# Performance work log

Hardware: AMD Instinct MI355X
Metric: run time of the kernel (lower is better)

The kernel has to match this reference:

```python
import jax, jax.numpy as jnp
import numpy as np

N = 50000        # nodes
E = 800000       # edges
IN_DIM, HID, OUT = 512, 256, 128
EPS = 1e-5       # PyG LayerNorm eps (added to std)


def setup_inputs() -> dict:
    key = jax.random.key(0)
    ks = jax.random.split(key, 24)
    def lin(k, i, o, scale=0.05):
        kw, kb = jax.random.split(k)
        return (jax.random.normal(kw, (i, o), jnp.float32) * scale,
                jax.random.normal(kb, (o,), jnp.float32) * scale)
    x = jax.random.normal(ks[0], (N, IN_DIM), jnp.float32)
    edge_index = jax.random.randint(ks[1], (2, E), 0, N, jnp.int64)
    Wq1, bq1 = lin(ks[2], IN_DIM, HID)
    Wk1, bk1 = lin(ks[3], IN_DIM, HID)
    Wv1, bv1 = lin(ks[4], IN_DIM, HID)
    Ws1, bs1 = lin(ks[5], IN_DIM, HID)
    g1 = jnp.ones((HID,), jnp.float32)
    be1 = jnp.zeros((HID,), jnp.float32)
    Wq2, bq2 = lin(ks[6], HID, OUT)
    Wk2, bk2 = lin(ks[7], HID, OUT)
    Wv2, bv2 = lin(ks[8], HID, OUT)
    Ws2, bs2 = lin(ks[9], HID, OUT)
    g2 = jnp.ones((OUT,), jnp.float32)
    be2 = jnp.zeros((OUT,), jnp.float32)
    return dict(x=x, Wq1=Wq1, bq1=bq1, Wk1=Wk1, bk1=bk1, Wv1=Wv1, bv1=bv1,
                Ws1=Ws1, bs1=bs1, g1=g1, be1=be1,
                Wq2=Wq2, bq2=bq2, Wk2=Wk2, bk2=bk2, Wv2=Wv2, bv2=bv2,
                Ws2=Ws2, bs2=bs2, g2=g2, be2=be2, edge_index=edge_index)


def transformer_conv(x, edge_index, Wq, bq, Wk, bk, Wv, bv, Ws, bs):
    # PyG TransformerConv, heads=1, concat=True, root_weight=True
    src, dst = edge_index[0], edge_index[1]
    n = x.shape[0]
    d = Wq.shape[1]
    q = x @ Wq + bq                               # [N, d]
    k = x @ Wk + bk
    v = x @ Wv + bv
    score = (q[dst] * k[src]).sum(-1) / jnp.sqrt(jnp.asarray(d, x.dtype))  # [E]
    m = jax.ops.segment_max(score, dst, num_segments=n)     # per-target max
    e = jnp.exp(score - m[dst])
    denom = jax.ops.segment_sum(e, dst, num_segments=n)
    alpha = e / denom[dst]                         # scatter-softmax over in-edges
    agg = jax.ops.segment_sum(alpha[:, None] * v[src], dst, num_segments=n)
    return agg + (x @ Ws + bs)                     # root/skip connection


def graph_layer_norm(h, w, b):
    # PyG LayerNorm mode='graph', no batch: normalize over ALL entries
    h = h - h.mean()
    return h / (h.std() + EPS) * w + b


def reference(x, Wq1, bq1, Wk1, bk1, Wv1, bv1, Ws1, bs1, g1, be1,
              Wq2, bq2, Wk2, bk2, Wv2, bv2, Ws2, bs2, g2, be2, edge_index):
    a1 = graph_layer_norm(
        transformer_conv(x, edge_index, Wq1, bq1, Wk1, bk1, Wv1, bv1, Ws1, bs1),
        g1, be1)
    h1 = jax.nn.elu(a1)  # ELU(alpha=1.0)
    h2 = graph_layer_norm(
        transformer_conv(h1, edge_index, Wq2, bq2, Wk2, bk2, Wv2, bv2, Ws2, bs2),
        g2, be2)
    return h2
```

## Files before the change

### kernel.cpp

```cpp
#include <hip/hip_runtime.h>
#include <stdint.h>
#include <math.h>

#define IN_DIM 512
#define HID    256
#define OUTD   128
#define LN_EPS 1e-5f
#define NSLOT  2048

typedef unsigned short u16;
typedef unsigned int   u32;
typedef short short8 __attribute__((ext_vector_type(8)));
typedef float f32x4  __attribute__((ext_vector_type(4)));

__device__ __forceinline__ float bf2f(u32 h) {
  union { u32 u; float f; } c; c.u = h << 16; return c.f;
}
__device__ __forceinline__ u16 f2bf(float f) {
  union { float f; u32 u; } c; c.f = f;
  u32 u = c.u;
  return (u16)((u + 0x7FFFu + ((u >> 16) & 1u)) >> 16);
}

__device__ __forceinline__ void gload_lds16(const void* g, void* l) {
  __builtin_amdgcn_global_load_lds((const __attribute__((address_space(1))) void*)g,
                                   (__attribute__((address_space(3))) void*)l, 16, 0, 0);
}

__global__ __launch_bounds__(256) void k_prep(
    const float* __restrict__ x, u16* __restrict__ x_bf, int n4,
    const int* __restrict__ edst, int* __restrict__ deg, int E,
    const float* __restrict__ bq1, const float* __restrict__ bk1,
    const float* __restrict__ bv1, const float* __restrict__ bs1,
    const float* __restrict__ bq2, const float* __restrict__ bk2,
    const float* __restrict__ bv2, const float* __restrict__ bs2,
    float* __restrict__ bc1, float* __restrict__ bc2,
    const float* __restrict__ Wq1, const float* __restrict__ Wk1,
    const float* __restrict__ Wv1, const float* __restrict__ Ws1,
    const float* __restrict__ Wq2, const float* __restrict__ Wk2,
    const float* __restrict__ Wv2, const float* __restrict__ Ws2,
    u16* __restrict__ Wt1, u16* __restrict__ Wt2,
    int b_cvt, int b_hist) {
  __shared__ u16 t[32][33];
  int blk = blockIdx.x;
  int tid = threadIdx.x;
  if (blk < b_cvt) {
    int id = blk * 256 + tid;
    if (id < n4) {
      const float4 v = ((const float4*)x)[id];
      ushort4 o;
      o.x = f2bf(v.x); o.y = f2bf(v.y); o.z = f2bf(v.z); o.w = f2bf(v.w);
      ((ushort4*)x_bf)[id] = o;
    }
    return;
  }
  blk -= b_cvt;
  if (blk < b_hist) {
    int e = blk * 256 + tid;
    if (e < E) atomicAdd(&deg[edst[e]], 1);
    return;
  }
  blk -= b_hist;
  if (blk < 6) {
    int id = blk * 256 + tid;
    if (id < 4 * HID) {
      const float* s = (id < HID) ? bq1 : (id < 2 * HID) ? bk1 : (id < 3 * HID) ? bv1 : bs1;
      bc1[id] = s[id & (HID - 1)];
    } else if (id < 4 * HID + 4 * OUTD) {
      int j = id - 4 * HID;
      const float* s = (j < OUTD) ? bq2 : (j < 2 * OUTD) ? bk2 : (j < 3 * OUTD) ? bv2 : bs2;
      bc2[j] = s[j & (OUTD - 1)];
    }
    return;
  }
  blk -= 6;
  int tx = tid & 31, ty = tid >> 5;
  if (blk < 512) {
    int mat = blk >> 7, r = blk & 127;
    int k0 = (r >> 3) * 32, n0 = (r & 7) * 32;
    const float* src = (mat == 0) ? Wq1 : (mat == 1) ? Wk1 : (mat == 2) ? Wv1 : Ws1;
    u16* dst = Wt1 + (size_t)mat * IN_DIM * HID;
#pragma unroll
    for (int i = 0; i < 32; i += 8)
      t[ty + i][tx] = f2bf(src[(size_t)(k0 + ty + i) * HID + n0 + tx]);
    __syncthreads();
#pragma unroll
    for (int i = 0; i < 32; i += 8)
      dst[(size_t)(n0 + ty + i) * IN_DIM + k0 + tx] = t[tx][ty + i];
    return;
  }
  blk -= 512;
  {
    int mat = blk >> 5, r = blk & 31;
    int k0 = (r >> 2) * 32, n0 = (r & 3) * 32;
    const float* src = (mat == 0) ? Wq2 : (mat == 1) ? Wk2 : (mat == 2) ? Wv2 : Ws2;
    u16* dst = Wt2 + (size_t)mat * HID * OUTD;
#pragma unroll
    for (int i = 0; i < 32; i += 8)
      t[ty + i][tx] = f2bf(src[(size_t)(k0 + ty + i) * OUTD + n0 + tx]);
    __syncthreads();
#pragma unroll
    for (int i = 0; i < 32; i += 8)
      dst[(size_t)(n0 + ty + i) * HID + k0 + tx] = t[tx][ty + i];
  }
}

__global__ void k_block_sum(const int* __restrict__ deg, int* __restrict__ bsum, int n) {
  __shared__ int sm[256];
  int i = blockIdx.x * 256 + threadIdx.x;
  sm[threadIdx.x] = (i < n) ? deg[i] : 0;
  __syncthreads();
  for (int off = 128; off > 0; off >>= 1) {
    if (threadIdx.x < off) sm[threadIdx.x] += sm[threadIdx.x + off];
    __syncthreads();
  }
  if (threadIdx.x == 0) bsum[blockIdx.x] = sm[0];
}

__global__ void k_scan_bsum(const int* __restrict__ bsum, int* __restrict__ boff, int nb) {
  __shared__ int sm[256];
  int t = threadIdx.x;
  int v = (t < nb) ? bsum[t] : 0;
  sm[t] = v;
  __syncthreads();
  for (int off = 1; off < 256; off <<= 1) {
    int tmp = (t >= off) ? sm[t - off] : 0;
    __syncthreads();
    sm[t] += tmp;
    __syncthreads();
  }
  if (t < nb) boff[t] = sm[t] - v;
}

__global__ void k_scan_final(const int* __restrict__ deg, const int* __restrict__ boff,
                             int* __restrict__ offsets, int* __restrict__ cur,
                             int n, int total) {
  __shared__ int sm[256];
  int t = threadIdx.x;
  int i = blockIdx.x * 256 + t;
  int v = (i < n) ? deg[i] : 0;
  sm[t] = v;
  __syncthreads();
  for (int off = 1; off < 256; off <<= 1) {
    int tmp = (t >= off) ? sm[t - off] : 0;
    __syncthreads();
    sm[t] += tmp;
    __syncthreads();
  }
  if (i < n) {
    int o = boff[blockIdx.x] + sm[t] - v;
    offsets[i] = o;
    cur[i] = o;
  }
  if (i == 0) offsets[n] = total;
}

__global__ void k_scatter(const int* __restrict__ src, const int* __restrict__ dst,
                          int* __restrict__ cursor, int* __restrict__ ssrc, int E) {
  int e = blockIdx.x * blockDim.x + threadIdx.x;
  if (e >= E) return;
  int d = dst[e];
  int pos = atomicAdd(&cursor[d], 1);
  ssrc[pos] = src[e];
}

__global__ __launch_bounds__(256, 2) void k_gemm_bf16_nt(
    const u16* __restrict__ A, const u16* __restrict__ Bt, const float* __restrict__ bias,
    u16* __restrict__ C, int M, int K, int Nt) {
  __shared__ __align__(16) u16 As[128 * 32];
  __shared__ __align__(16) u16 Bs[256 * 32];
  const int tid = threadIdx.x;
  const int bm0 = blockIdx.x * 128;
  const int bn0 = blockIdx.y * 256;
  const int wave = tid >> 6, lane = tid & 63;
  const int q = lane >> 4, r16 = lane & 15;
  const int wm = (wave >> 1) * 64;
  const int wn = (wave & 1) * 128;

  f32x4 acc[4][8];
#pragma unroll
  for (int i = 0; i < 4; i++)
#pragma unroll
    for (int j = 0; j < 8; j++) acc[i][j] = (f32x4){0.f, 0.f, 0.f, 0.f};

  for (int kt = 0; kt < K; kt += 32) {
#pragma unroll
    for (int j = 0; j < 2; ++j) {
      int t = j * 256 + tid;
      gload_lds16(A + (size_t)(bm0 + (t >> 2)) * K + kt + (t & 3) * 8, &As[t * 8]);
    }
#pragma unroll
    for (int j = 0; j < 4; ++j) {
      int t = j * 256 + tid;
      gload_lds16(Bt + (size_t)(bn0 + (t >> 2)) * K + kt + (t & 3) * 8, &Bs[t * 8]);
    }
    __syncthreads();
    short8 bfr[8];
#pragma unroll
    for (int j = 0; j < 8; ++j)
      bfr[j] = *(const short8*)(&Bs[(wn + j * 16 + r16) * 32 + q * 8]);
#pragma unroll
    for (int i = 0; i < 4; ++i) {
      short8 af = *(const short8*)(&As[(wm + i * 16 + r16) * 32 + q * 8]);
#pragma unroll
      for (int j = 0; j < 8; ++j)
        acc[i][j] = __builtin_amdgcn_mfma_f32_16x16x32_bf16(af, bfr[j], acc[i][j], 0, 0, 0);
    }
    __syncthreads();
  }

#pragma unroll
  for (int i = 0; i < 4; i++) {
#pragma unroll
    for (int r = 0; r < 4; r++) {
      int grow = bm0 + wm + i * 16 + q * 4 + r;
      if (grow >= M) continue;
      size_t rbase = (size_t)grow * Nt;
#pragma unroll
      for (int j = 0; j < 8; j++) {
        int gcol = bn0 + wn + j * 16 + r16;
        float v = acc[i][j][r] + bias[gcol];
        C[rbase + gcol] = f2bf(v);
      }
    }
  }
}

template <int VPL>
__device__ __forceinline__ void load_bf(const u16* __restrict__ p, int lane, float* f) {
  if constexpr (VPL == 4) {
    uint2 r = *(const uint2*)(p + lane * 4);
    f[0] = bf2f(r.x & 0xffffu); f[1] = bf2f(r.x >> 16);
    f[2] = bf2f(r.y & 0xffffu); f[3] = bf2f(r.y >> 16);
  } else {
    u32 r = *(const u32*)(p + lane * 2);
    f[0] = bf2f(r & 0xffffu); f[1] = bf2f(r >> 16);
  }
}

template <int H, bool OUT_BF16>
__global__ __launch_bounds__(256) void k_conv(
    const u16* __restrict__ qkvs, const int* __restrict__ offsets,
    const int* __restrict__ ssrc, u16* __restrict__ out_bf,
    float* __restrict__ out_f, int n, float scale,
    float* __restrict__ ssum, float* __restrict__ ssq) {
  constexpr int VPL = H / 64;
  int gw = (blockIdx.x * blockDim.x + threadIdx.x) >> 6;
  int wave = threadIdx.x >> 6;
  int lane = threadIdx.x & 63;
  if (gw >= n) return;
  const u16* base = qkvs + (size_t)gw * (4 * H);
  float qf[VPL];
  load_bf<VPL>(base, lane, qf);
  int beg = offsets[gw], end = offsets[gw + 1];
  float m = -INFINITY, l = 0.f;
  float agg[VPL];
#pragma unroll
  for (int w = 0; w < VPL; w++) agg[w] = 0.f;

  int i = beg;
  for (; i + 4 <= end; i += 4) {
    int s0 = ssrc[i], s1 = ssrc[i + 1], s2 = ssrc[i + 2], s3 = ssrc[i + 3];
    const u16* k0p = qkvs + (size_t)s0 * (4 * H) + H;
    const u16* k1p = qkvs + (size_t)s1 * (4 * H) + H;
    const u16* k2p = qkvs + (size_t)s2 * (4 * H) + H;
    const u16* k3p = qkvs + (size_t)s3 * (4 * H) + H;
    float k0[VPL], k1[VPL], k2[VPL], k3[VPL];
    float v0[VPL], v1[VPL], v2[VPL], v3[VPL];
    load_bf<VPL>(k0p, lane, k0);
    load_bf<VPL>(k1p, lane, k1);
    load_bf<VPL>(k2p, lane, k2);
    load_bf<VPL>(k3p, lane, k3);
    load_bf<VPL>(k0p + H, lane, v0);
    load_bf<VPL>(k1p + H, lane, v1);
    load_bf<VPL>(k2p + H, lane, v2);
    load_bf<VPL>(k3p + H, lane, v3);
    float d0 = 0.f, d1 = 0.f, d2 = 0.f, d3 = 0.f;
#pragma unroll
    for (int w = 0; w < VPL; w++) {
      d0 += qf[w] * k0[w]; d1 += qf[w] * k1[w];
      d2 += qf[w] * k2[w]; d3 += qf[w] * k3[w];
    }
#pragma unroll
    for (int off = 32; off > 0; off >>= 1) {
      d0 += __shfl_xor(d0, off, 64);
      d1 += __shfl_xor(d1, off, 64);
      d2 += __shfl_xor(d2, off, 64);
      d3 += __shfl_xor(d3, off, 64);
    }
    d0 *= scale; d1 *= scale; d2 *= scale; d3 *= scale;
    float cm = fmaxf(fmaxf(d0, d1), fmaxf(d2, d3));
    float nm = fmaxf(m, cm);
    float sc = __expf(m - nm);
    float p0 = __expf(d0 - nm), p1 = __expf(d1 - nm);
    float p2 = __expf(d2 - nm), p3 = __expf(d3 - nm);
    m = nm;
    l = l * sc + (p0 + p1) + (p2 + p3);
#pragma unroll
    for (int w = 0; w < VPL; w++)
      agg[w] = agg[w] * sc + p0 * v0[w] + p1 * v1[w] + p2 * v2[w] + p3 * v3[w];
  }
  for (; i < end; ++i) {
    int s = ssrc[i];
    const u16* kb = qkvs + (size_t)s * (4 * H) + H;
    float kf[VPL], vf[VPL];
    load_bf<VPL>(kb, lane, kf);
    load_bf<VPL>(kb + H, lane, vf);
    float d = 0.f;
#pragma unroll
    for (int w = 0; w < VPL; w++) d += qf[w] * kf[w];
#pragma unroll
    for (int off = 32; off > 0; off >>= 1) d += __shfl_xor(d, off, 64);
    float score = d * scale;
    float nm = fmaxf(m, score);
    float sc = __expf(m - nm);
    float p = __expf(score - nm);
    m = nm;
    l = l * sc + p;
#pragma unroll
    for (int w = 0; w < VPL; w++) agg[w] = agg[w] * sc + p * vf[w];
  }

  float sf[VPL];
  load_bf<VPL>(base + 3 * H, lane, sf);
  float inv = (end > beg) ? 1.f / l : 0.f;
  float r[VPL];
#pragma unroll
  for (int w = 0; w < VPL; w++) {
    r[w] = agg[w] * inv + sf[w];
    if (OUT_BF16) out_bf[(size_t)gw * H + lane * VPL + w] = f2bf(r[w]);
    else out_f[(size_t)gw * H + lane * VPL + w] = r[w];
  }

  float s = 0.f, s2 = 0.f;
#pragma unroll
  for (int w = 0; w < VPL; w++) { s += r[w]; s2 += r[w] * r[w]; }
#pragma unroll
  for (int off = 32; off > 0; off >>= 1) {
    s += __shfl_xor(s, off, 64);
    s2 += __shfl_xor(s2, off, 64);
  }
  if (lane == 0) {
    int slot = (blockIdx.x * 4 + wave) & (NSLOT - 1);
    atomicAdd(&ssum[slot], s);
    atomicAdd(&ssq[slot], s2);
  }
}

__device__ __forceinline__ void slot_stats(const float* __restrict__ ssum,
                                           const float* __restrict__ ssq,
                                           double cnt, float& mu, float& inv) {
  __shared__ double rs[256], rq[256];
  double ls = 0.0, lq = 0.0;
  for (int i = threadIdx.x; i < NSLOT; i += 256) {
    ls += (double)ssum[i];
    lq += (double)ssq[i];
  }
  rs[threadIdx.x] = ls; rq[threadIdx.x] = lq;
  __syncthreads();
  for (int off = 128; off > 0; off >>= 1) {
    if (threadIdx.x < off) { rs[threadIdx.x] += rs[threadIdx.x + off]; rq[threadIdx.x] += rq[threadIdx.x + off]; }
    __syncthreads();
  }
  double mud = rs[0] / cnt;
  double var = rq[0] / cnt - mud * mud;
  if (var < 0.0) var = 0.0;
  mu = (float)mud;
  inv = (float)(1.0 / (sqrt(var) + (double)LN_EPS));
}

__global__ __launch_bounds__(256) void k_norm_elu_bf16(
    const u16* __restrict__ a, const float* __restrict__ g,
    const float* __restrict__ b, const float* __restrict__ ssum,
    const float* __restrict__ ssq, double cnt,
    u16* __restrict__ out, int n8, int Hmask) {
  float mu, inv;
  slot_stats(ssum, ssq, cnt, mu, inv);
  int id = blockIdx.x * blockDim.x + threadIdx.x;
  if (id >= n8) return;
  int i8 = id * 8;
  int cb = i8 & Hmask;
  uint4 v = *(const uint4*)(a + i8);
  const u32 va[4] = {v.x, v.y, v.z, v.w};
  uint4 o;
  u32* op = (u32*)&o;
#pragma unroll
  for (int w = 0; w < 4; w++) {
    float y0 = (bf2f(va[w] & 0xffffu) - mu) * inv * g[cb + 2 * w] + b[cb + 2 * w];
    float y1 = (bf2f(va[w] >> 16) - mu) * inv * g[cb + 2 * w + 1] + b[cb + 2 * w + 1];
    y0 = (y0 > 0.f) ? y0 : (__expf(y0) - 1.f);
    y1 = (y1 > 0.f) ? y1 : (__expf(y1) - 1.f);
    op[w] = (u32)f2bf(y0) | ((u32)f2bf(y1) << 16);
  }
  *(uint4*)(out + i8) = o;
}

__global__ __launch_bounds__(256) void k_norm_f32(
    float* __restrict__ a, const float* __restrict__ g,
    const float* __restrict__ b, const float* __restrict__ ssum,
    const float* __restrict__ ssq, double cnt, int n4, int Hmask) {
  float mu, inv;
  slot_stats(ssum, ssq, cnt, mu, inv);
  int id = blockIdx.x * blockDim.x + threadIdx.x;
  if (id >= n4) return;
  int i4 = id * 4;
  int cb = i4 & Hmask;
  float4 v = *(const float4*)(a + i4);
  float4 o;
  o.x = (v.x - mu) * inv * g[cb] + b[cb];
  o.y = (v.y - mu) * inv * g[cb + 1] + b[cb + 1];
  o.z = (v.z - mu) * inv * g[cb + 2] + b[cb + 2];
  o.w = (v.w - mu) * inv * g[cb + 3] + b[cb + 3];
  *(float4*)(a + i4) = o;
}

extern "C" void kernel_launch(void* const* d_in, const int* in_sizes, int n_in,
                              void* d_out, int out_size, void* d_ws, size_t ws_size,
                              hipStream_t stream) {
  const float* x   = (const float*)d_in[0];
  const float* Wq1 = (const float*)d_in[1];  const float* bq1 = (const float*)d_in[2];
  const float* Wk1 = (const float*)d_in[3];  const float* bk1 = (const float*)d_in[4];
  const float* Wv1 = (const float*)d_in[5];  const float* bv1 = (const float*)d_in[6];
  const float* Ws1 = (const float*)d_in[7];  const float* bs1 = (const float*)d_in[8];
  const float* g1  = (const float*)d_in[9];  const float* be1 = (const float*)d_in[10];
  const float* Wq2 = (const float*)d_in[11]; const float* bq2 = (const float*)d_in[12];
  const float* Wk2 = (const float*)d_in[13]; const float* bk2 = (const float*)d_in[14];
  const float* Wv2 = (const float*)d_in[15]; const float* bv2 = (const float*)d_in[16];
  const float* Ws2 = (const float*)d_in[17]; const float* bs2 = (const float*)d_in[18];
  const float* g2  = (const float*)d_in[19]; const float* be2 = (const float*)d_in[20];
  const int*   ei  = (const int*)d_in[21];

  const int N = in_sizes[0] / IN_DIM;
  const int E = in_sizes[21] / 2;
  const int* esrc = ei;
  const int* edst = ei + E;

  char* w = (char*)d_ws;
  auto carve = [&](size_t bytes) { char* p = w; w += (bytes + 255) & ~(size_t)255; return p; };
  int* deg     = (int*)carve((size_t)(N + 1) * 4);
  float* slots = (float*)carve(4 * NSLOT * 4);
  u16* x_bf  = (u16*)carve((size_t)N * IN_DIM * 2);
  u16* Wt1   = (u16*)carve((size_t)4 * HID * IN_DIM * 2);
  u16* Wt2   = (u16*)carve((size_t)4 * OUTD * HID * 2);
  float* bc1 = (float*)carve(4 * HID * 4);
  float* bc2 = (float*)carve(4 * OUTD * 4);
  u16* qkvs1 = (u16*)carve((size_t)N * 4 * HID * 2);
  u16* a1    = (u16*)carve((size_t)N * HID * 2);
  int* offs  = (int*)carve((size_t)(N + 1) * 4);
  int* cur   = (int*)carve((size_t)(N + 1) * 4);
  int* ssrc  = (int*)carve((size_t)E * 4);
  int* bsum  = (int*)carve(1024);
  int* boff  = (int*)carve(1024);
  u16* h1    = x_bf;
  u16* qkvs2 = qkvs1;
  float* ssum1 = slots, *ssq1 = slots + NSLOT;
  float* ssum2 = slots + 2 * NSLOT, *ssq2 = slots + 3 * NSLOT;

  hipMemsetAsync(deg, 0, (size_t)((char*)(slots + 4 * NSLOT) - (char*)deg), stream);

  int n4 = N * IN_DIM / 4;
  int b_cvt = (n4 + 255) / 256;
  int b_hist = (E + 255) / 256;
  int k1_blocks = b_cvt + b_hist + 6 + 512 + 128;
  k_prep<<<k1_blocks, 256, 0, stream>>>(
      x, x_bf, n4, edst, deg, E,
      bq1, bk1, bv1, bs1, bq2, bk2, bv2, bs2, bc1, bc2,
      Wq1, Wk1, Wv1, Ws1, Wq2, Wk2, Wv2, Ws2, Wt1, Wt2, b_cvt, b_hist);

  int nb = (N + 255) / 256;
  k_block_sum<<<nb, 256, 0, stream>>>(deg, bsum, N);
  k_scan_bsum<<<1, 256, 0, stream>>>(bsum, boff, nb);
  k_scan_final<<<nb, 256, 0, stream>>>(deg, boff, offs, cur, N, E);

  k_scatter<<<b_hist, 256, 0, stream>>>(esrc, edst, cur, ssrc, E);

  dim3 gg1((N + 127) / 128, (4 * HID) / 256);
  k_gemm_bf16_nt<<<gg1, 256, 0, stream>>>(x_bf, Wt1, bc1, qkvs1, N, IN_DIM, 4 * HID);

  k_conv<HID, true><<<(N + 3) / 4, 256, 0, stream>>>(qkvs1, offs, ssrc, a1, nullptr, N,
                                                     1.0f / sqrtf((float)HID), ssum1, ssq1);
  k_norm_elu_bf16<<<N * HID / 8 / 256, 256, 0, stream>>>(
      a1, g1, be1, ssum1, ssq1, (double)N * HID, h1, N * HID / 8, HID - 1);

  dim3 gg2((N + 127) / 128, (4 * OUTD) / 256);
  k_gemm_bf16_nt<<<gg2, 256, 0, stream>>>(h1, Wt2, bc2, qkvs2, N, HID, 4 * OUTD);

  k_conv<OUTD, false><<<(N + 3) / 4, 256, 0, stream>>>(qkvs2, offs, ssrc, nullptr, (float*)d_out,
                                                       N, 1.0f / sqrtf((float)OUTD), ssum2, ssq2);
  k_norm_f32<<<N * OUTD / 4 / 256, 256, 0, stream>>>(
      (float*)d_out, g2, be2, ssum2, ssq2, (double)N * OUTD, N * OUTD / 4, OUTD - 1);
}
```

Measured before the change: 622.9 us.

## Quantize gathered K/V to int8 per-node and fuse edge scatter into GEMM launch

The GEMM epilogue now splits its output into separate Q/S and K/V buffers. A new quantization kernel converts K (and V in layer 1) to int8 with a per-node, per-section scale. The conv kernels gather these int8 rows instead of bf16, which halves the bytes read per edge in the bandwidth-bound attention aggregation. The CSR edge scatter is folded into the layer-1 GEMM launch as extra blocks, removing one kernel launch. This trades accuracy for less gather traffic and adds extra quantize passes plus a wider output write.

```diff
diff --git a/kernel.cpp b/kernel.cpp
--- a/kernel.cpp
+++ b/kernel.cpp
@@ -10,6 +10,7 @@
 
 typedef unsigned short u16;
 typedef unsigned int   u32;
+typedef unsigned char  u8;
 typedef short short8 __attribute__((ext_vector_type(8)));
 typedef float f32x4  __attribute__((ext_vector_type(4)));
 
@@ -20,6 +21,10 @@
   union { float f; u32 u; } c; c.f = f;
   u32 u = c.u;
   return (u16)((u + 0x7FFFu + ((u >> 16) & 1u)) >> 16);
+}
+template <int W>
+__device__ __forceinline__ float i8f(u32 word) {
+  return (float)((int)(word << (24 - 8 * W)) >> 24);
 }
 
 __device__ __forceinline__ void gload_lds16(const void* g, void* l) {
@@ -155,23 +160,27 @@
   if (i == 0) offsets[n] = total;
 }
 
-__global__ void k_scatter(const int* __restrict__ src, const int* __restrict__ dst,
-                          int* __restrict__ cursor, int* __restrict__ ssrc, int E) {
-  int e = blockIdx.x * blockDim.x + threadIdx.x;
-  if (e >= E) return;
-  int d = dst[e];
-  int pos = atomicAdd(&cursor[d], 1);
-  ssrc[pos] = src[e];
-}
-
-__global__ __launch_bounds__(256, 2) void k_gemm_bf16_nt(
+__global__ __launch_bounds__(256, 2) void k_gemm(
     const u16* __restrict__ A, const u16* __restrict__ Bt, const float* __restrict__ bias,
-    u16* __restrict__ C, int M, int K, int Nt) {
+    u16* __restrict__ Cb, u16* __restrict__ Ck,
+    int M, int K, int Nt, int mbx, int cklo, int ckhi, int sB, int sK,
+    int gemm_blocks,
+    const int* __restrict__ esrc, const int* __restrict__ edst,
+    int* __restrict__ cur, int* __restrict__ ssrc, int E) {
+  if ((int)blockIdx.x >= gemm_blocks) {
+    int e = (blockIdx.x - gemm_blocks) * 256 + threadIdx.x;
+    if (e < E) {
+      int d = edst[e];
+      int pos = atomicAdd(&cur[d], 1);
+      ssrc[pos] = esrc[e];
+    }
+    return;
+  }
   __shared__ __align__(16) u16 As[128 * 32];
   __shared__ __align__(16) u16 Bs[256 * 32];
   const int tid = threadIdx.x;
-  const int bm0 = blockIdx.x * 128;
-  const int bn0 = blockIdx.y * 256;
+  const int bm0 = (blockIdx.x % mbx) * 128;
+  const int bn0 = (blockIdx.x / mbx) * 256;
   const int wave = tid >> 6, lane = tid & 63;
   const int q = lane >> 4, r16 = lane & 15;
   const int wm = (wave >> 1) * 64;
@@ -209,78 +218,133 @@
     __syncthreads();
   }
 
+  const int wk = ckhi - cklo;
 #pragma unroll
   for (int i = 0; i < 4; i++) {
 #pragma unroll
     for (int r = 0; r < 4; r++) {
       int grow = bm0 + wm + i * 16 + q * 4 + r;
       if (grow >= M) continue;
-      size_t rbase = (size_t)grow * Nt;
 #pragma unroll
       for (int j = 0; j < 8; j++) {
         int gcol = bn0 + wn + j * 16 + r16;
         float v = acc[i][j][r] + bias[gcol];
-        C[rbase + gcol] = f2bf(v);
+        if (gcol < cklo) Cb[(size_t)grow * sB + gcol] = f2bf(v);
+        else if (gcol < ckhi) Ck[(size_t)grow * sK + gcol - cklo] = f2bf(v);
+        else Cb[(size_t)grow * sB + gcol - wk] = f2bf(v);
       }
     }
   }
 }
 
-template <int VPL>
-__device__ __forceinline__ void load_bf(const u16* __restrict__ p, int lane, float* f) {
+template <int SECW, int NSEC>
+__global__ __launch_bounds__(256) void k_quant(
+    const u16* __restrict__ src, u8* __restrict__ dst,
+    float* __restrict__ sc, int n) {
+  constexpr int VPL = SECW / 64;
+  int gw = (blockIdx.x * blockDim.x + threadIdx.x) >> 6;
+  int lane = threadIdx.x & 63;
+  int node = gw / NSEC, sec = gw - node * NSEC;
+  if (node >= n) return;
+  const u16* p = src + (size_t)node * (NSEC * SECW) + sec * SECW + lane * VPL;
+  float f[VPL];
   if constexpr (VPL == 4) {
-    uint2 r = *(const uint2*)(p + lane * 4);
+    uint2 r = *(const uint2*)p;
     f[0] = bf2f(r.x & 0xffffu); f[1] = bf2f(r.x >> 16);
     f[2] = bf2f(r.y & 0xffffu); f[3] = bf2f(r.y >> 16);
   } else {
-    u32 r = *(const u32*)(p + lane * 2);
+    u32 r = *(const u32*)p;
     f[0] = bf2f(r & 0xffffu); f[1] = bf2f(r >> 16);
   }
-}
-
-template <int H, bool OUT_BF16>
+  float amax = 0.f;
+#pragma unroll
+  for (int w = 0; w < VPL; w++) amax = fmaxf(amax, fabsf(f[w]));
+#pragma unroll
+  for (int off = 32; off > 0; off >>= 1) amax = fmaxf(amax, __shfl_xor(amax, off, 64));
+  float rs = (amax > 0.f) ? 127.0f / amax : 0.f;
+  u32 packed = 0;
+#pragma unroll
+  for (int w = 0; w < VPL; w++) {
+    int qv = (int)rintf(f[w] * rs);
+    packed |= ((u32)(qv & 0xff)) << (8 * w);
+  }
+  u8* d = dst + (size_t)node * (NSEC * SECW) + sec * SECW + lane * VPL;
+  if constexpr (VPL == 4) *(u32*)d = packed;
+  else *(u16*)d = (u16)packed;
+  if (lane == 0) sc[node * NSEC + sec] = amax / 127.0f;
+}
+
+template <int H, bool OUT_BF16, bool V_I8>
 __global__ __launch_bounds__(256) void k_conv(
-    const u16* __restrict__ qkvs, const int* __restrict__ offsets,
-    const int* __restrict__ ssrc, u16* __restrict__ out_bf,
-    float* __restrict__ out_f, int n, float scale,
+    const u16* __restrict__ qs, const u8* __restrict__ k8,
+    const float* __restrict__ sc,
+    const int* __restrict__ offsets, const int* __restrict__ ssrc,
+    u16* __restrict__ out_bf, float* __restrict__ out_f, int n, float scale,
     float* __restrict__ ssum, float* __restrict__ ssq) {
   constexpr int VPL = H / 64;
+  constexpr int QSTR = V_I8 ? 2 * H : 3 * H;
+  constexpr int SOFF = V_I8 ? H : 2 * H;
+  constexpr int KSTR = V_I8 ? 2 * H : H;
   int gw = (blockIdx.x * blockDim.x + threadIdx.x) >> 6;
   int wave = threadIdx.x >> 6;
   int lane = threadIdx.x & 63;
   if (gw >= n) return;
-  const u16* base = qkvs + (size_t)gw * (4 * H);
+  const u16* base = qs + (size_t)gw * QSTR;
   float qf[VPL];
-  load_bf<VPL>(base, lane, qf);
+  if constexpr (VPL == 4) {
+    uint2 rq = *(const uint2*)(base + lane * 4);
+    qf[0] = bf2f(rq.x & 0xffffu); qf[1] = bf2f(rq.x >> 16);
+    qf[2] = bf2f(rq.y & 0xffffu); qf[3] = bf2f(rq.y >> 16);
+  } else {
+    u32 rq = *(const u32*)(base + lane * 2);
+    qf[0] = bf2f(rq & 0xffffu); qf[1] = bf2f(rq >> 16);
+  }
   int beg = offsets[gw], end = offsets[gw + 1];
   float m = -INFINITY, l = 0.f;
   float agg[VPL];
 #pragma unroll
   for (int w = 0; w < VPL; w++) agg[w] = 0.f;
 
+  auto kload = [&](int s) -> u32 {
+    const u8* kp = k8 + (size_t)s * KSTR;
+    if constexpr (VPL == 4) return *(const u32*)(kp + lane * 4);
+    else return (u32)*(const u16*)(kp + lane * 2);
+  };
+  auto vload = [&](int s) -> u32 {
+    if constexpr (V_I8) return *(const u32*)(k8 + (size_t)s * KSTR + H + lane * 4);
+    else return *(const u32*)(qs + (size_t)s * QSTR + H + lane * 2);
+  };
+  auto vload2 = [&](int s) -> u32 {
+    return 0u;
+  };
+  (void)vload2;
+  auto dotk = [&](u32 kq) -> float {
+    float d = 0.f;
+    d += qf[0] * i8f<0>(kq);
+    d += qf[1] * i8f<1>(kq);
+    if constexpr (VPL == 4) {
+      d += qf[2] * i8f<2>(kq);
+      d += qf[3] * i8f<3>(kq);
+    }
+    return d;
+  };
+
   int i = beg;
   for (; i + 4 <= end; i += 4) {
     int s0 = ssrc[i], s1 = ssrc[i + 1], s2 = ssrc[i + 2], s3 = ssrc[i + 3];
-    const u16* k0p = qkvs + (size_t)s0 * (4 * H) + H;
-    const u16* k1p = qkvs + (size_t)s1 * (4 * H) + H;
-    const u16* k2p = qkvs + (size_t)s2 * (4 * H) + H;
-    const u16* k3p = qkvs + (size_t)s3 * (4 * H) + H;
-    float k0[VPL], k1[VPL], k2[VPL], k3[VPL];
-    float v0[VPL], v1[VPL], v2[VPL], v3[VPL];
-    load_bf<VPL>(k0p, lane, k0);
-    load_bf<VPL>(k1p, lane, k1);
-    load_bf<VPL>(k2p, lane, k2);
-    load_bf<VPL>(k3p, lane, k3);
-    load_bf<VPL>(k0p + H, lane, v0);
-    load_bf<VPL>(k1p + H, lane, v1);
-    load_bf<VPL>(k2p + H, lane, v2);
-    load_bf<VPL>(k3p + H, lane, v3);
-    float d0 = 0.f, d1 = 0.f, d2 = 0.f, d3 = 0.f;
-#pragma unroll
-    for (int w = 0; w < VPL; w++) {
-      d0 += qf[w] * k0[w]; d1 += qf[w] * k1[w];
-      d2 += qf[w] * k2[w]; d3 += qf[w] * k3[w];
-    }
+    u32 kq0 = kload(s0), kq1 = kload(s1), kq2 = kload(s2), kq3 = kload(s3);
+    u32 v0 = vload(s0), v1 = vload(s1), v2 = vload(s2), v3 = vload(s3);
+    float ks0, ks1, ks2, ks3, vs0, vs1, vs2, vs3;
+    if constexpr (V_I8) {
+      float2 a0 = *(const float2*)(sc + s0 * 2), a1 = *(const float2*)(sc + s1 * 2);
+      float2 a2 = *(const float2*)(sc + s2 * 2), a3 = *(const float2*)(sc + s3 * 2);
+      ks0 = a0.x; vs0 = a0.y; ks1 = a1.x; vs1 = a1.y;
+      ks2 = a2.x; vs2 = a2.y; ks3 = a3.x; vs3 = a3.y;
+    } else {
+      ks0 = sc[s0]; ks1 = sc[s1]; ks2 = sc[s2]; ks3 = sc[s3];
+      vs0 = vs1 = vs2 = vs3 = 1.f;
+    }
+    float d0 = dotk(kq0), d1 = dotk(kq1), d2 = dotk(kq2), d3 = dotk(kq3);
 #pragma unroll
     for (int off = 32; off > 0; off >>= 1) {
       d0 += __shfl_xor(d0, off, 64);
@@ -288,41 +352,74 @@
       d2 += __shfl_xor(d2, off, 64);
       d3 += __shfl_xor(d3, off, 64);
     }
-    d0 *= scale; d1 *= scale; d2 *= scale; d3 *= scale;
+    d0 *= scale * ks0; d1 *= scale * ks1; d2 *= scale * ks2; d3 *= scale * ks3;
     float cm = fmaxf(fmaxf(d0, d1), fmaxf(d2, d3));
     float nm = fmaxf(m, cm);
-    float sc = __expf(m - nm);
+    float sfac = __expf(m - nm);
     float p0 = __expf(d0 - nm), p1 = __expf(d1 - nm);
     float p2 = __expf(d2 - nm), p3 = __expf(d3 - nm);
     m = nm;
-    l = l * sc + (p0 + p1) + (p2 + p3);
-#pragma unroll
-    for (int w = 0; w < VPL; w++)
-      agg[w] = agg[w] * sc + p0 * v0[w] + p1 * v1[w] + p2 * v2[w] + p3 * v3[w];
+    l = l * sfac + (p0 + p1) + (p2 + p3);
+    if constexpr (V_I8) { p0 *= vs0; p1 *= vs1; p2 *= vs2; p3 *= vs3; }
+#pragma unroll
+    for (int w = 0; w < VPL; w++) {
+      float f0, f1, f2v, f3;
+      if constexpr (V_I8) {
+        f0 = (w == 0) ? i8f<0>(v0) : (w == 1) ? i8f<1>(v0) : (w == 2) ? i8f<2>(v0) : i8f<3>(v0);
+        f1 = (w == 0) ? i8f<0>(v1) : (w == 1) ? i8f<1>(v1) : (w == 2) ? i8f<2>(v1) : i8f<3>(v1);
+        f2v = (w == 0) ? i8f<0>(v2) : (w == 1) ? i8f<1>(v2) : (w == 2) ? i8f<2>(v2) : i8f<3>(v2);
+        f3 = (w == 0) ? i8f<0>(v3) : (w == 1) ? i8f<1>(v3) : (w == 2) ? i8f<2>(v3) : i8f<3>(v3);
+      } else {
+        u32 sh = 16 * (w & 1);
+        f0 = bf2f((v0 >> sh) & 0xffffu);
+        f1 = bf2f((v1 >> sh) & 0xffffu);
+        f2v = bf2f((v2 >> sh) & 0xffffu);
+        f3 = bf2f((v3 >> sh) & 0xffffu);
+      }
+      agg[w] = agg[w] * sfac + p0 * f0 + p1 * f1 + p2 * f2v + p3 * f3;
+    }
   }
   for (; i < end; ++i) {
     int s = ssrc[i];
-    const u16* kb = qkvs + (size_t)s * (4 * H) + H;
-    float kf[VPL], vf[VPL];
-    load_bf<VPL>(kb, lane, kf);
-    load_bf<VPL>(kb + H, lane, vf);
-    float d = 0.f;
-#pragma unroll
-    for (int w = 0; w < VPL; w++) d += qf[w] * kf[w];
+    u32 kq = kload(s);
+    u32 vr = vload(s);
+    float ks, vs;
+    if constexpr (V_I8) {
+      float2 a = *(const float2*)(sc + s * 2);
+      ks = a.x; vs = a.y;
+    } else { ks = sc[s]; vs = 1.f; }
+    float d = dotk(kq);
 #pragma unroll
     for (int off = 32; off > 0; off >>= 1) d += __shfl_xor(d, off, 64);
-    float score = d * scale;
+    float score = d * scale * ks;
     float nm = fmaxf(m, score);
-    float sc = __expf(m - nm);
+    float sfac = __expf(m - nm);
     float p = __expf(score - nm);
     m = nm;
-    l = l * sc + p;
-#pragma unroll
-    for (int w = 0; w < VPL; w++) agg[w] = agg[w] * sc + p * vf[w];
+    l = l * sfac + p;
+    float pv = V_I8 ? p * vs : p;
+#pragma unroll
+    for (int w = 0; w < VPL; w++) {
+      float vf;
+      if constexpr (V_I8)
+        vf = (w == 0) ? i8f<0>(vr) : (w == 1) ? i8f<1>(vr) : (w == 2) ? i8f<2>(vr) : i8f<3>(vr);
+      else vf = bf2f((vr >> (16 * (w & 1))) & 0xffffu);
+      agg[w] = agg[w] * sfac + pv * vf;
+    }
   }
 
   float sf[VPL];
-  load_bf<VPL>(base + 3 * H, lane, sf);
+  {
+    const u16* sp = base + SOFF;
+    if constexpr (VPL == 4) {
+      uint2 rs = *(const uint2*)(sp + lane * 4);
+      sf[0] = bf2f(rs.x & 0xffffu); sf[1] = bf2f(rs.x >> 16);
+      sf[2] = bf2f(rs.y & 0xffffu); sf[3] = bf2f(rs.y >> 16);
+    } else {
+      u32 rs = *(const u32*)(sp + lane * 2);
+      sf[0] = bf2f(rs & 0xffffu); sf[1] = bf2f(rs >> 16);
+    }
+  }
   float inv = (end > beg) ? 1.f / l : 0.f;
   float r[VPL];
 #pragma unroll
@@ -444,7 +541,10 @@
   u16* Wt2   = (u16*)carve((size_t)4 * OUTD * HID * 2);
   float* bc1 = (float*)carve(4 * HID * 4);
   float* bc2 = (float*)carve(4 * OUTD * 4);
-  u16* qkvs1 = (u16*)carve((size_t)N * 4 * HID * 2);
+  u16* qs1   = (u16*)carve((size_t)N * 2 * HID * 2);
+  u16* kvt   = (u16*)carve((size_t)N * 2 * HID * 2);
+  u8*  kv8   = (u8*)carve((size_t)N * 2 * HID);
+  float* sc1 = (float*)carve((size_t)N * 2 * 4);
   u16* a1    = (u16*)carve((size_t)N * HID * 2);
   int* offs  = (int*)carve((size_t)(N + 1) * 4);
   int* cur   = (int*)carve((size_t)(N + 1) * 4);
@@ -452,7 +552,10 @@
   int* bsum  = (int*)carve(1024);
   int* boff  = (int*)carve(1024);
   u16* h1    = x_bf;
-  u16* qkvs2 = qkvs1;
+  u16* qvs2  = qs1;
+  u16* ktmp2 = kvt;
+  u8*  k82   = kv8;
+  float* sc2 = sc1;
   float* ssum1 = slots, *ssq1 = slots + NSLOT;
   float* ssum2 = slots + 2 * NSLOT, *ssq2 = slots + 3 * NSLOT;
 
@@ -472,21 +575,33 @@
   k_scan_bsum<<<1, 256, 0, stream>>>(bsum, boff, nb);
   k_scan_final<<<nb, 256, 0, stream>>>(deg, boff, offs, cur, N, E);
 
-  k_scatter<<<b_hist, 256, 0, stream>>>(esrc, edst, cur, ssrc, E);
-
-  dim3 gg1((N + 127) / 128, (4 * HID) / 256);
-  k_gemm_bf16_nt<<<gg1, 256, 0, stream>>>(x_bf, Wt1, bc1, qkvs1, N, IN_DIM, 4 * HID);
-
-  k_conv<HID, true><<<(N + 3) / 4, 256, 0, stream>>>(qkvs1, offs, ssrc, a1, nullptr, N,
-                                                     1.0f / sqrtf((float)HID), ssum1, ssq1);
+  int mbx = (N + 127) / 128;
+  int g1_blocks = mbx * ((4 * HID) / 256);
+  k_gemm<<<g1_blocks + b_hist, 256, 0, stream>>>(
+      x_bf, Wt1, bc1, qs1, kvt, N, IN_DIM, 4 * HID, mbx,
+      HID, 3 * HID, 2 * HID, 2 * HID, g1_blocks,
+      esrc, edst, cur, ssrc, E);
+
+  k_quant<HID, 2><<<(N * 2 + 3) / 4, 256, 0, stream>>>(kvt, kv8, sc1, N);
+
+  k_conv<HID, true, true><<<(N + 3) / 4, 256, 0, stream>>>(
+      qs1, kv8, sc1, offs, ssrc, a1, nullptr, N, 1.0f / sqrtf((float)HID), ssum1, ssq1);
+
   k_norm_elu_bf16<<<N * HID / 8 / 256, 256, 0, stream>>>(
       a1, g1, be1, ssum1, ssq1, (double)N * HID, h1, N * HID / 8, HID - 1);
 
-  dim3 gg2((N + 127) / 128, (4 * OUTD) / 256);
-  k_gemm_bf16_nt<<<gg2, 256, 0, stream>>>(h1, Wt2, bc2, qkvs2, N, HID, 4 * OUTD);
-
-  k_conv<OUTD, false><<<(N + 3) / 4, 256, 0, stream>>>(qkvs2, offs, ssrc, nullptr, (float*)d_out,
-                                                       N, 1.0f / sqrtf((float)OUTD), ssum2, ssq2);
+  int g2_blocks = mbx * ((4 * OUTD) / 256);
+  k_gemm<<<g2_blocks, 256, 0, stream>>>(
+      h1, Wt2, bc2, qvs2, ktmp2, N, HID, 4 * OUTD, mbx,
+      OUTD, 2 * OUTD, 3 * OUTD, OUTD, g2_blocks,
+      nullptr, nullptr, nullptr, nullptr, 0);
+
+  k_quant<OUTD, 1><<<(N + 3) / 4, 256, 0, stream>>>(ktmp2, k82, sc2, N);
+
+  k_conv<OUTD, false, false><<<(N + 3) / 4, 256, 0, stream>>>(
+      qvs2, k82, sc2, offs, ssrc, nullptr, (float*)d_out, N,
+      1.0f / sqrtf((float)OUTD), ssum2, ssq2);
+
   k_norm_f32<<<N * OUTD / 4 / 256, 256, 0, stream>>>(
       (float*)d_out, g2, be2, ssum2, ssq2, (double)N * OUTD, N * OUTD / 4, OUTD - 1);
 }
```

After: 672.7 us. 1.08x slower.
